# Kernel tuning notes

Hardware: AMD Instinct MI355X
Metric: run time of the kernel (lower is better)

Reference implementation:

```python
import jax, jax.numpy as jnp
import numpy as np

N_ITERS = 10
LAMBDA0 = 0.01


def skew(p):
    # p: (..., 3) -> (..., 3, 3) skew-symmetric matrices
    x, y, z = p[..., 0], p[..., 1], p[..., 2]
    O = jnp.zeros_like(x)
    return jnp.stack([O, -z, y, z, O, -x, -y, x, O], -1).reshape(p.shape[:-1] + (3, 3))


def so3exp(w):
    # Rodrigues formula for a single (3,) rotation vector
    theta2 = jnp.sum(w * w)
    theta = jnp.sqrt(theta2 + 1e-24)
    small = theta < 1e-4
    a = jnp.where(small, 1.0 - theta2 / 6.0, jnp.sin(theta) / theta)
    b = jnp.where(small, 0.5 - theta2 / 24.0, (1.0 - jnp.cos(theta)) / (theta2 + 1e-24))
    W = skew(w)
    return jnp.eye(3, dtype=w.dtype) + a * W + b * (W @ W)


def gather_feats(fm, p2, width, height):
    # fm: (C, Hf, Wf); p2: (N, 2) int pixel coords (x, y). Mirrors indexing_ with
    # flipped points: row = floor(y*Hf/height), col = floor(x*Wf/width).
    Hf, Wf = fm.shape[1], fm.shape[2]
    rows = jnp.clip((p2[:, 1] * Hf) // height, 0, Hf - 1)
    cols = jnp.clip((p2[:, 0] * Wf) // width, 0, Wf - 1)
    return fm[:, rows, cols].T  # (N, C)


def project(pts3D, R, t, K):
    p3 = pts3D @ R.T + t                                  # (N, 3) camera frame
    proj = p3 @ K.T
    xy = jnp.clip(proj[:, :2] / proj[:, 2:3], -1e6, 1e6)  # from_homogeneous
    p2 = jnp.round(xy).astype(jnp.int32) - 1              # (N, 2) int pixels
    return p3, p2


def support_mask(p2, width, height):
    return (p2[:, 0] >= 0) & (p2[:, 1] >= 0) & (p2[:, 0] < width) & (p2[:, 1] < height)


def masked_mean_cost(fm, feature_ref, p2, mask, width, height):
    err = gather_feats(fm, p2, width, height) - feature_ref
    m = mask.astype(err.dtype)
    c = 0.5 * jnp.sum(err * err, -1) * m
    return jnp.sum(c) / jnp.maximum(jnp.sum(m), 1.0)


def setup_inputs():
    key = jax.random.key(0)
    ks = jax.random.split(key, 7)
    N, C, Hf, Wf = 50000, 128, 480, 640
    z = jax.random.uniform(ks[0], (N,), minval=4.0, maxval=8.0)
    x = jax.random.uniform(ks[1], (N,), minval=-0.4, maxval=0.4) * z
    y = jax.random.uniform(ks[2], (N,), minval=-0.3, maxval=0.3) * z
    pts3D = jnp.stack([x, y, z], -1).astype(jnp.float32)
    feature_map_query = jax.random.normal(ks[3], (C, Hf, Wf), jnp.float32)
    feature_grad_x = 0.1 * jax.random.normal(ks[4], (C, Hf, Wf), jnp.float32)
    feature_grad_y = 0.1 * jax.random.normal(ks[5], (C, Hf, Wf), jnp.float32)
    feature_ref = jax.random.normal(ks[6], (N, C), jnp.float32)
    K = jnp.array([[600.0, 0.0, 320.0], [0.0, 600.0, 240.0], [0.0, 0.0, 1.0]], jnp.float32)
    R_init = jnp.eye(3, dtype=jnp.float32)
    t_init = jnp.array([0.1, 0.1, 0.0], jnp.float32)
    return dict(pts3D=pts3D, feature_ref=feature_ref, feature_map_query=feature_map_query,
                feature_grad_x=feature_grad_x, feature_grad_y=feature_grad_y, K=K,
                R_init=R_init, t_init=t_init, im_width=640, im_height=480)


def reference(pts3D, feature_ref, feature_map_query, feature_grad_x, feature_grad_y,
              K, R_init, t_init, im_width, im_height):
    N = pts3D.shape[0]
    fx, fy = K[0, 0], K[1, 1]
    R, t = R_init, t_init
    lam = jnp.asarray(LAMBDA0, pts3D.dtype)
    lr = jnp.asarray(1.0, pts3D.dtype)
    lr_reset = 1.0

    # initial cost (prev_cost at iteration 0 in the original)
    _, p2_0 = project(pts3D, R, t, K)
    mask0 = support_mask(p2_0, im_width, im_height)
    prev_cost = masked_mean_cost(feature_map_query, feature_ref, p2_0, mask0, im_width, im_height)

    eyeN = jnp.broadcast_to(jnp.eye(3, dtype=pts3D.dtype), (N, 3, 3))

    for _ in range(N_ITERS):
        p3, p2 = project(pts3D, R, t, K)
        mask = support_mask(p2, im_width, im_height)
        m = mask.astype(pts3D.dtype)

        err = gather_feats(feature_map_query, p2, im_width, im_height) - feature_ref  # (N, C)

        Z = p3[:, 2]
        Zs = jnp.where(jnp.abs(Z) > 1e-6, Z, 1e-6)  # guard masked-out points only
        # J_p_T: d p3 / d [t, w]  -> (N, 3, 6)
        J_p_T = jnp.concatenate([eyeN, -skew(p3)], -1)
        o = jnp.ones_like(Zs)
        zz = jnp.zeros_like(Zs)
        # J_px_p: d pixel / d p3 -> (N, 2, 3)
        J_px_p = jnp.stack([fx * o, zz, -fx * p3[:, 0] / Zs,
                            zz, fy * o, -fy * p3[:, 1] / Zs], -1).reshape(N, 2, 3) / Zs[:, None, None]
        gx = gather_feats(feature_grad_x, p2, im_width, im_height)  # (N, C)
        gy = gather_feats(feature_grad_y, p2, im_width, im_height)
        J_f_px = jnp.stack([gx, gy], -1)            # (N, C, 2)
        J = J_f_px @ (J_px_p @ J_p_T)               # (N, C, 6)
        Jm = J * m[:, None, None]                   # zero out unsupported points

        Grad = jnp.einsum('ncj,nc->j', Jm, err)     # (6,)
        Hess = jnp.einsum('nck,ncl->kl', Jm, Jm)    # (6, 6)

        Hd = Hess + lam * jnp.diag(jnp.diagonal(Hess) + 1e-9)
        delta = -lr * (jnp.linalg.inv(Hd) @ Grad)
        dt, dw = delta[:3], delta[3:6]
        dr = so3exp(dw)
        R_new = dr @ R
        t_new = dr @ t + dt

        _, p2n = project(pts3D, R_new, t_new, K)
        maskn = support_mask(p2n, im_width, im_height)
        new_cost = masked_mean_cost(feature_map_query, feature_ref, p2n, maskn, im_width, im_height)

        accept = new_cost <= prev_cost
        lam = jnp.clip(lam * jnp.where(accept, 0.1, 10.0), 1e-6, 1e4)
        lr = jnp.where(accept, lr_reset, jnp.clip(0.1 * lr, 1e-3, 1.0))
        R = jnp.where(accept, R_new, R)
        t = jnp.where(accept, t_new, t)
        prev_cost = jnp.where(accept, new_cost, prev_cost)

    return R, t
```

## Files before the change

### kernel.cpp

```cpp
#include <hip/hip_runtime.h>
#include <math.h>

#define NCH 128
#define IMW 640
#define IMH 480
#define HW (IMW * IMH)
#define THREADS 512
#define WPB (THREADS / 64)
#define GBLK 512
#define TSTRIDE (3 * NCH)

#define S_R    0
#define S_T    9
#define S_RC   12
#define S_TC   21
#define S_LAM  24
#define S_LR   25
#define S_PREV 26
#define S_G    32
#define S_TOTAL 64

#define PCOLS 29

struct ProjR {
  float x, y, z;
  int pix;
  bool m;
};

__device__ __forceinline__ ProjR project_pt(const float* __restrict__ pts, int n,
                                            const float R[9], const float T[3],
                                            const float Kv[9]) {
  float px = pts[3 * n + 0], py = pts[3 * n + 1], pz = pts[3 * n + 2];
  ProjR o;
  o.x = R[0] * px + R[1] * py + R[2] * pz + T[0];
  o.y = R[3] * px + R[4] * py + R[5] * pz + T[1];
  o.z = R[6] * px + R[7] * py + R[8] * pz + T[2];
  float pr0 = Kv[0] * o.x + Kv[1] * o.y + Kv[2] * o.z;
  float pr1 = Kv[3] * o.x + Kv[4] * o.y + Kv[5] * o.z;
  float pr2 = Kv[6] * o.x + Kv[7] * o.y + Kv[8] * o.z;
  float u = fminf(fmaxf(pr0 / pr2, -1000000.0f), 1000000.0f);
  float v = fminf(fmaxf(pr1 / pr2, -1000000.0f), 1000000.0f);
  int p2x = (int)rintf(u) - 1;
  int p2y = (int)rintf(v) - 1;
  o.m = (p2x >= 0) && (p2y >= 0) && (p2x < IMW) && (p2y < IMH);
  int r = min(max(p2y, 0), IMH - 1);
  int c = min(max(p2x, 0), IMW - 1);
  o.pix = r * IMW + c;
  return o;
}

__device__ __forceinline__ void jac_rows(const ProjR& p, float fx, float fy,
                                         float A0[6], float A1[6]) {
  float Zs = (fabsf(p.z) > 1e-6f) ? p.z : 1e-6f;
  float iz = 1.0f / Zs;
  float j00 = fx * iz;
  float j02 = -fx * p.x * iz * iz;
  float j11 = fy * iz;
  float j12 = -fy * p.y * iz * iz;
  A0[0] = j00; A0[1] = 0.0f; A0[2] = j02;
  A0[3] = j02 * p.y; A0[4] = j00 * p.z - j02 * p.x; A0[5] = -j00 * p.y;
  A1[0] = 0.0f; A1[1] = j11; A1[2] = j12;
  A1[3] = -j11 * p.z + j12 * p.y; A1[4] = -j12 * p.x; A1[5] = j11 * p.x;
}

__global__ void init_kernel(const float* __restrict__ Rin,
                            const float* __restrict__ tin,
                            double* __restrict__ st) {
  int i = threadIdx.x;
  if (i < 9) { st[S_R + i] = (double)Rin[i]; st[S_RC + i] = (double)Rin[i]; }
  if (i < 3) { st[S_T + i] = (double)tin[i]; st[S_TC + i] = (double)tin[i]; }
  if (i == 0) { st[S_LAM] = 0.01; st[S_LR] = 1.0; st[S_PREV] = 0.0; }
}

__global__ __launch_bounds__(256) void transpose3_kernel(
    const float* __restrict__ f, const float* __restrict__ gx,
    const float* __restrict__ gy, float* __restrict__ t) {
  __shared__ float4 tile4[64][32];
  const int map = blockIdx.y;
  const float* in = (map == 0) ? f : (map == 1) ? gx : gy;
  const int pix0 = blockIdx.x * 64;
#pragma unroll
  for (int mm = 0; mm < 8; ++mm) {
    int k = threadIdx.x + 256 * mm;
    int c  = k >> 4;
    int p4 = (k & 15) * 4;
    float4 v = ((const float4*)(in + (size_t)c * HW + pix0))[k & 15];
    int sw = (c >> 2) ^ (k & 15);
    int e  = c & 3;
    ((float*)&tile4[p4 + 0][sw])[e] = v.x;
    ((float*)&tile4[p4 + 1][sw])[e] = v.y;
    ((float*)&tile4[p4 + 2][sw])[e] = v.z;
    ((float*)&tile4[p4 + 3][sw])[e] = v.w;
  }
  __syncthreads();
#pragma unroll
  for (int mm = 0; mm < 8; ++mm) {
    int k = threadIdx.x + 256 * mm;
    int px = k >> 5;
    int c4 = k & 31;
    float4 v = tile4[px][c4 ^ (px >> 2)];
    ((float4*)(t + (size_t)(pix0 + px) * TSTRIDE + (size_t)map * NCH))[c4] = v;
  }
}

template <bool TRANS>
__global__ __launch_bounds__(THREADS) void fused_kernel(
    const float* __restrict__ pts, const float* __restrict__ fref,
    const float* __restrict__ mf, const float* __restrict__ mgx,
    const float* __restrict__ mgy, const float* __restrict__ Kmat,
    const double* __restrict__ st, double* __restrict__ part, int N) {
  const int lane = threadIdx.x & 63;
  const int wib  = threadIdx.x >> 6;
  const int gw = blockIdx.x * WPB + wib;
  const int nw = gridDim.x * WPB;
  const int half = lane >> 5;
  const int hl   = lane & 31;

  float R[9], T[3], Kv[9];
#pragma unroll
  for (int i = 0; i < 9; ++i) { R[i] = (float)st[S_RC + i]; Kv[i] = Kmat[i]; }
#pragma unroll
  for (int i = 0; i < 3; ++i) T[i] = (float)st[S_TC + i];
  const float fx = Kv[0], fy = Kv[4];

  float hacc[27];
#pragma unroll
  for (int j = 0; j < 27; ++j) hacc[j] = 0.0f;
  double csum = 0.0;
  float cntf = 0.0f;

  for (int base = gw * 2; base < N; base += 2 * nw) {
    const int n = base + half;
    const int nc = min(n, N - 1);
    ProjR p = project_pt(pts, nc, R, T, Kv);
    const float m = (p.m && n < N) ? 1.0f : 0.0f;
    if (__all(m == 0.0f)) continue;

    float A0[6], A1[6];
    jac_rows(p, fx, fy, A0, A1);

    float e0, e1, e2, e3;
    float gxx, gxy, gyy, gxe, gye;
    if (TRANS) {
      const float4* t4 = (const float4*)mf;
      const size_t b = (size_t)p.pix * (TSTRIDE / 4) + hl;
      float4 fv = t4[b];
      float4 gv = t4[b + 32];
      float4 hv = t4[b + 64];
      float4 rv = ((const float4*)fref)[(size_t)nc * (NCH / 4) + hl];
      e0 = fv.x - rv.x; e1 = fv.y - rv.y; e2 = fv.z - rv.z; e3 = fv.w - rv.w;
      gxx = gv.x * gv.x + gv.y * gv.y + gv.z * gv.z + gv.w * gv.w;
      gxy = gv.x * hv.x + gv.y * hv.y + gv.z * hv.z + gv.w * hv.w;
      gyy = hv.x * hv.x + hv.y * hv.y + hv.z * hv.z + hv.w * hv.w;
      gxe = gv.x * e0 + gv.y * e1 + gv.z * e2 + gv.w * e3;
      gye = hv.x * e0 + hv.y * e1 + hv.z * e2 + hv.w * e3;
    } else {
      const int c0 = hl * 4;
      const size_t bb = (size_t)p.pix;
      float f0 = mf[(size_t)(c0 + 0) * HW + bb];
      float f1 = mf[(size_t)(c0 + 1) * HW + bb];
      float f2 = mf[(size_t)(c0 + 2) * HW + bb];
      float f3 = mf[(size_t)(c0 + 3) * HW + bb];
      float gx0 = mgx[(size_t)(c0 + 0) * HW + bb];
      float gx1 = mgx[(size_t)(c0 + 1) * HW + bb];
      float gx2 = mgx[(size_t)(c0 + 2) * HW + bb];
      float gx3 = mgx[(size_t)(c0 + 3) * HW + bb];
      float gy0 = mgy[(size_t)(c0 + 0) * HW + bb];
      float gy1 = mgy[(size_t)(c0 + 1) * HW + bb];
      float gy2 = mgy[(size_t)(c0 + 2) * HW + bb];
      float gy3 = mgy[(size_t)(c0 + 3) * HW + bb];
      float4 rv = ((const float4*)fref)[(size_t)nc * (NCH / 4) + hl];
      e0 = f0 - rv.x; e1 = f1 - rv.y; e2 = f2 - rv.z; e3 = f3 - rv.w;
      gxx = gx0 * gx0 + gx1 * gx1 + gx2 * gx2 + gx3 * gx3;
      gxy = gx0 * gy0 + gx1 * gy1 + gx2 * gy2 + gx3 * gy3;
      gyy = gy0 * gy0 + gy1 * gy1 + gy2 * gy2 + gy3 * gy3;
      gxe = gx0 * e0 + gx1 * e1 + gx2 * e2 + gx3 * e3;
      gye = gy0 * e0 + gy1 * e1 + gy2 * e2 + gy3 * e3;
    }

    gxx *= m; gxy *= m; gyy *= m; gxe *= m; gye *= m;
    csum += (double)(m * (e0 * e0 + e1 * e1 + e2 * e2 + e3 * e3));
    if (hl == 0) cntf += m;

#pragma unroll
    for (int k = 0; k < 6; ++k) hacc[k] += gxe * A0[k] + gye * A1[k];
    float u[6], v[6];
#pragma unroll
    for (int k = 0; k < 6; ++k) {
      u[k] = gxx * A0[k] + gxy * A1[k];
      v[k] = gxy * A0[k] + gyy * A1[k];
    }
    int q = 6;
#pragma unroll
    for (int k = 0; k < 6; ++k)
#pragma unroll
      for (int l = k; l < 6; ++l) {
        hacc[q] += u[k] * A0[l] + v[k] * A1[l];
        ++q;
      }
  }

  __shared__ double red[WPB][PCOLS];
#pragma unroll
  for (int j = 0; j < 27; ++j) {
    double d = (double)hacc[j];
#pragma unroll
    for (int off = 32; off > 0; off >>= 1) d += __shfl_xor(d, off);
    if (lane == 0) red[wib][j] = d;
  }
  {
    double cs = csum;
    float cf = cntf;
#pragma unroll
    for (int off = 32; off > 0; off >>= 1) {
      cs += __shfl_xor(cs, off);
      cf += __shfl_xor(cf, off);
    }
    if (lane == 0) { red[wib][27] = cs; red[wib][28] = (double)cf; }
  }
  __syncthreads();
  if (wib == 0 && lane < PCOLS) {
    double s = 0.0;
#pragma unroll
    for (int w = 0; w < WPB; ++w) s += red[w][lane];
    part[(size_t)blockIdx.x * PCOLS + lane] = s;
  }
}

__global__ void update_solve_kernel(const double* __restrict__ part, int GB,
                                    double* __restrict__ st,
                                    float* __restrict__ out, int is_init) {
  __shared__ double red[16][PCOLS];
  __shared__ double tot[PCOLS];
  int q = threadIdx.x & 31;
  int chunk = threadIdx.x >> 5;
  if (q < PCOLS) {
    double s = 0.0;
    for (int b = chunk; b < GB; b += 16) s += part[(size_t)b * PCOLS + q];
    red[chunk][q] = s;
  }
  __syncthreads();
  if (threadIdx.x < PCOLS) {
    double t = 0.0;
#pragma unroll
    for (int ch = 0; ch < 16; ++ch) t += red[ch][threadIdx.x];
    tot[threadIdx.x] = t;
  }
  __syncthreads();
  if (threadIdx.x == 0) {
    double nc = 0.5 * tot[27] / fmax(tot[28], 1.0);
    bool accept;
    if (is_init) {
      accept = true;
      st[S_PREV] = nc;
    } else {
      accept = (nc <= st[S_PREV]);
      double lam = st[S_LAM] * (accept ? 0.1 : 10.0);
      st[S_LAM] = fmin(fmax(lam, 1e-6), 1e4);
      st[S_LR] = accept ? 1.0 : fmin(fmax(0.1 * st[S_LR], 1e-3), 1.0);
      if (accept) st[S_PREV] = nc;
    }
    if (accept) {
      for (int i = 0; i < 9; ++i) st[S_R + i] = st[S_RC + i];
      for (int i = 0; i < 3; ++i) st[S_T + i] = st[S_TC + i];
      for (int j = 0; j < 27; ++j) st[S_G + j] = tot[j];
    }
    for (int i = 0; i < 9; ++i) out[i] = (float)st[S_R + i];
    for (int i = 0; i < 3; ++i) out[9 + i] = (float)st[S_T + i];

    double Grad[6], Hs[6][6];
    for (int j = 0; j < 6; ++j) Grad[j] = st[S_G + j];
    int qq = 0;
    for (int k = 0; k < 6; ++k)
      for (int l = k; l < 6; ++l) { Hs[k][l] = Hs[l][k] = st[S_G + 6 + qq]; ++qq; }
    double lam = st[S_LAM], lr = st[S_LR];
    double M[6][7];
    for (int i = 0; i < 6; ++i) {
      for (int j = 0; j < 6; ++j) M[i][j] = Hs[i][j];
      M[i][i] += lam * (Hs[i][i] + 1e-9);
      M[i][6] = Grad[i];
    }
    for (int c = 0; c < 6; ++c) {
      int piv = c;
      double mx = fabs(M[c][c]);
      for (int r = c + 1; r < 6; ++r) {
        double a = fabs(M[r][c]);
        if (a > mx) { mx = a; piv = r; }
      }
      if (piv != c)
        for (int j = 0; j < 7; ++j) {
          double tmp = M[c][j]; M[c][j] = M[piv][j]; M[piv][j] = tmp;
        }
      double pv = M[c][c];
      if (pv == 0.0) pv = 1e-30;
      for (int r = c + 1; r < 6; ++r) {
        double f = M[r][c] / pv;
        for (int j = c; j < 7; ++j) M[r][j] -= f * M[c][j];
      }
    }
    double xs[6];
    for (int i = 5; i >= 0; --i) {
      double v = M[i][6];
      for (int j = i + 1; j < 6; ++j) v -= M[i][j] * xs[j];
      double pv = M[i][i];
      if (pv == 0.0) pv = 1e-30;
      xs[i] = v / pv;
    }
    double dt[3] = {-lr * xs[0], -lr * xs[1], -lr * xs[2]};
    double dw[3] = {-lr * xs[3], -lr * xs[4], -lr * xs[5]};
    double th2 = dw[0] * dw[0] + dw[1] * dw[1] + dw[2] * dw[2];
    double th = sqrt(th2 + 1e-24);
    double a, b;
    if (th < 1e-4) { a = 1.0 - th2 / 6.0; b = 0.5 - th2 / 24.0; }
    else { a = sin(th) / th; b = (1.0 - cos(th)) / (th2 + 1e-24); }
    double W[3][3] = {{0, -dw[2], dw[1]}, {dw[2], 0, -dw[0]}, {-dw[1], dw[0], 0}};
    double W2[3][3];
    for (int i = 0; i < 3; ++i)
      for (int j = 0; j < 3; ++j) {
        double s = 0.0;
        for (int k = 0; k < 3; ++k) s += W[i][k] * W[k][j];
        W2[i][j] = s;
      }
    double dr[3][3];
    for (int i = 0; i < 3; ++i)
      for (int j = 0; j < 3; ++j)
        dr[i][j] = ((i == j) ? 1.0 : 0.0) + a * W[i][j] + b * W2[i][j];
    for (int i = 0; i < 3; ++i) {
      for (int j = 0; j < 3; ++j) {
        double s = 0.0;
        for (int k = 0; k < 3; ++k) s += dr[i][k] * st[S_R + k * 3 + j];
        st[S_RC + i * 3 + j] = s;
      }
      double s = 0.0;
      for (int k = 0; k < 3; ++k) s += dr[i][k] * st[S_T + k];
      st[S_TC + i] = s + dt[i];
    }
  }
}

extern "C" void kernel_launch(void* const* d_in, const int* in_sizes, int n_in,
                              void* d_out, int out_size, void* d_ws, size_t ws_size,
                              hipStream_t stream) {
  const float* pts  = (const float*)d_in[0];
  const float* fref = (const float*)d_in[1];
  const float* fm   = (const float*)d_in[2];
  const float* gxm  = (const float*)d_in[3];
  const float* gym  = (const float*)d_in[4];
  const float* Kmat = (const float*)d_in[5];
  const float* Rin  = (const float*)d_in[6];
  const float* tin  = (const float*)d_in[7];
  const int N = in_sizes[0] / 3;

  double* st = (double*)d_ws;
  double* part = st + S_TOTAL;
  float* out = (float*)d_out;

  const size_t state_doubles = S_TOTAL + (size_t)GBLK * PCOLS;
  const size_t map_floats = (size_t)HW * NCH;
  const size_t need_fast =
      state_doubles * sizeof(double) + 3 * map_floats * sizeof(float) + 256;

  init_kernel<<<1, 64, 0, stream>>>(Rin, tin, st);

  if (ws_size >= need_fast) {
    float* tmap = (float*)(st + state_doubles);
    transpose3_kernel<<<dim3(HW / 64, 3), 256, 0, stream>>>(fm, gxm, gym, tmap);
    fused_kernel<true><<<GBLK, THREADS, 0, stream>>>(pts, fref, tmap, tmap, tmap,
                                                     Kmat, st, part, N);
    update_solve_kernel<<<1, 512, 0, stream>>>(part, GBLK, st, out, 1);
    for (int it = 0; it < 10; ++it) {
      fused_kernel<true><<<GBLK, THREADS, 0, stream>>>(pts, fref, tmap, tmap,
                                                       tmap, Kmat, st, part, N);
      update_solve_kernel<<<1, 512, 0, stream>>>(part, GBLK, st, out, 0);
    }
  } else {
    fused_kernel<false><<<GBLK, THREADS, 0, stream>>>(pts, fref, fm, gxm, gym,
                                                      Kmat, st, part, N);
    update_solve_kernel<<<1, 512, 0, stream>>>(part, GBLK, st, out, 1);
    for (int it = 0; it < 10; ++it) {
      fused_kernel<false><<<GBLK, THREADS, 0, stream>>>(pts, fref, fm, gxm, gym,
                                                        Kmat, st, part, N);
      update_solve_kernel<<<1, 512, 0, stream>>>(part, GBLK, st, out, 0);
    }
  }
}
```

Measured before the change: 1.033 ms.

## Sort points by projected pixel bucket to improve gather locality

Adds a counting sort (key, scan, scatter kernels) that orders points by their initial projected pixel bucket, and the fused kernel iterates through this order. The aim is for neighbouring waves to gather nearby rows of the transposed feature maps, improving cache hit rates. It also flattens the transpose grid so the three maps interleave. The cost is three extra launches, an indirection on each point, and scattered reads of points and reference features.

After: 1.064 ms. 1.03x slower.

```diff
diff --git a/kernel.cpp b/kernel.cpp
--- a/kernel.cpp
+++ b/kernel.cpp
@@ -9,6 +9,7 @@
 #define WPB (THREADS / 64)
 #define GBLK 512
 #define TSTRIDE (3 * NCH)
+#define NBUCK (HW / 64)
 
 #define S_R    0
 #define S_T    9
@@ -66,20 +67,80 @@
 
 __global__ void init_kernel(const float* __restrict__ Rin,
                             const float* __restrict__ tin,
-                            double* __restrict__ st) {
-  int i = threadIdx.x;
-  if (i < 9) { st[S_R + i] = (double)Rin[i]; st[S_RC + i] = (double)Rin[i]; }
-  if (i < 3) { st[S_T + i] = (double)tin[i]; st[S_TC + i] = (double)tin[i]; }
-  if (i == 0) { st[S_LAM] = 0.01; st[S_LR] = 1.0; st[S_PREV] = 0.0; }
+                            double* __restrict__ st, int* __restrict__ hist) {
+  if (blockIdx.x == 0) {
+    int i = threadIdx.x;
+    if (i < 9) { st[S_R + i] = (double)Rin[i]; st[S_RC + i] = (double)Rin[i]; }
+    if (i < 3) { st[S_T + i] = (double)tin[i]; st[S_TC + i] = (double)tin[i]; }
+    if (i == 0) { st[S_LAM] = 0.01; st[S_LR] = 1.0; st[S_PREV] = 0.0; }
+  }
+  int gid = blockIdx.x * blockDim.x + threadIdx.x;
+  for (int i = gid; i < NBUCK; i += gridDim.x * blockDim.x) hist[i] = 0;
+}
+
+__global__ __launch_bounds__(256) void sort_key_kernel(
+    const float* __restrict__ pts, const float* __restrict__ Rin,
+    const float* __restrict__ tin, const float* __restrict__ Kmat,
+    int* __restrict__ keys, int* __restrict__ hist, int N) {
+  int n = blockIdx.x * 256 + threadIdx.x;
+  if (n >= N) return;
+  float R[9], T[3], Kv[9];
+#pragma unroll
+  for (int i = 0; i < 9; ++i) { R[i] = Rin[i]; Kv[i] = Kmat[i]; }
+#pragma unroll
+  for (int i = 0; i < 3; ++i) T[i] = tin[i];
+  ProjR p = project_pt(pts, n, R, T, Kv);
+  keys[n] = p.pix;
+  atomicAdd(&hist[p.pix >> 6], 1);
+}
+
+__global__ __launch_bounds__(512) void sort_scan_kernel(
+    const int* __restrict__ hist, int* __restrict__ offs) {
+  __shared__ int tsum[512];
+  const int C = (NBUCK + 511) / 512;
+  int t = threadIdx.x;
+  int local[C];
+  int s = 0;
+#pragma unroll
+  for (int j = 0; j < C; ++j) {
+    int idx = t * C + j;
+    int v = (idx < NBUCK) ? hist[idx] : 0;
+    local[j] = s;
+    s += v;
+  }
+  tsum[t] = s;
+  __syncthreads();
+  for (int off = 1; off < 512; off <<= 1) {
+    int y = (t >= off) ? tsum[t - off] : 0;
+    __syncthreads();
+    tsum[t] += y;
+    __syncthreads();
+  }
+  int base = (t == 0) ? 0 : tsum[t - 1];
+#pragma unroll
+  for (int j = 0; j < C; ++j) {
+    int idx = t * C + j;
+    if (idx < NBUCK) offs[idx] = base + local[j];
+  }
+}
+
+__global__ __launch_bounds__(256) void sort_scatter_kernel(
+    const int* __restrict__ keys, int* __restrict__ offs,
+    int* __restrict__ order, int N) {
+  int n = blockIdx.x * 256 + threadIdx.x;
+  if (n >= N) return;
+  int b = keys[n] >> 6;
+  int pos = atomicAdd(&offs[b], 1);
+  order[pos] = n;
 }
 
 __global__ __launch_bounds__(256) void transpose3_kernel(
     const float* __restrict__ f, const float* __restrict__ gx,
     const float* __restrict__ gy, float* __restrict__ t) {
   __shared__ float4 tile4[64][32];
-  const int map = blockIdx.y;
+  const int map = blockIdx.x % 3;
+  const int pix0 = (blockIdx.x / 3) * 64;
   const float* in = (map == 0) ? f : (map == 1) ? gx : gy;
-  const int pix0 = blockIdx.x * 64;
 #pragma unroll
   for (int mm = 0; mm < 8; ++mm) {
     int k = threadIdx.x + 256 * mm;
@@ -109,6 +170,7 @@
     const float* __restrict__ pts, const float* __restrict__ fref,
     const float* __restrict__ mf, const float* __restrict__ mgx,
     const float* __restrict__ mgy, const float* __restrict__ Kmat,
+    const int* __restrict__ order,
     const double* __restrict__ st, double* __restrict__ part, int N) {
   const int lane = threadIdx.x & 63;
   const int wib  = threadIdx.x >> 6;
@@ -131,10 +193,10 @@
   float cntf = 0.0f;
 
   for (int base = gw * 2; base < N; base += 2 * nw) {
-    const int n = base + half;
-    const int nc = min(n, N - 1);
-    ProjR p = project_pt(pts, nc, R, T, Kv);
-    const float m = (p.m && n < N) ? 1.0f : 0.0f;
+    const int i = base + half;
+    const int n = order[min(i, N - 1)];
+    ProjR p = project_pt(pts, n, R, T, Kv);
+    const float m = (p.m && i < N) ? 1.0f : 0.0f;
     if (__all(m == 0.0f)) continue;
 
     float A0[6], A1[6];
@@ -148,7 +210,7 @@
       float4 fv = t4[b];
       float4 gv = t4[b + 32];
       float4 hv = t4[b + 64];
-      float4 rv = ((const float4*)fref)[(size_t)nc * (NCH / 4) + hl];
+      float4 rv = ((const float4*)fref)[(size_t)n * (NCH / 4) + hl];
       e0 = fv.x - rv.x; e1 = fv.y - rv.y; e2 = fv.z - rv.z; e3 = fv.w - rv.w;
       gxx = gv.x * gv.x + gv.y * gv.y + gv.z * gv.z + gv.w * gv.w;
       gxy = gv.x * hv.x + gv.y * hv.y + gv.z * hv.z + gv.w * hv.w;
@@ -170,7 +232,7 @@
       float gy1 = mgy[(size_t)(c0 + 1) * HW + bb];
       float gy2 = mgy[(size_t)(c0 + 2) * HW + bb];
       float gy3 = mgy[(size_t)(c0 + 3) * HW + bb];
-      float4 rv = ((const float4*)fref)[(size_t)nc * (NCH / 4) + hl];
+      float4 rv = ((const float4*)fref)[(size_t)n * (NCH / 4) + hl];
       e0 = f0 - rv.x; e1 = f1 - rv.y; e2 = f2 - rv.z; e3 = f3 - rv.w;
       gxx = gx0 * gx0 + gx1 * gx1 + gx2 * gx2 + gx3 * gx3;
       gxy = gx0 * gy0 + gx1 * gy1 + gx2 * gy2 + gx3 * gy3;
@@ -354,33 +416,45 @@
 
   double* st = (double*)d_ws;
   double* part = st + S_TOTAL;
+  int* keys  = (int*)(part + (size_t)GBLK * PCOLS);
+  int* order = keys + N;
+  int* hist  = order + N;
+  int* offs  = hist + NBUCK;
+  size_t int_end = (size_t)((char*)(offs + NBUCK) - (char*)d_ws);
+  size_t tmap_off = (int_end + 15) & ~(size_t)15;
+  float* tmap = (float*)((char*)d_ws + tmap_off);
   float* out = (float*)d_out;
 
-  const size_t state_doubles = S_TOTAL + (size_t)GBLK * PCOLS;
   const size_t map_floats = (size_t)HW * NCH;
-  const size_t need_fast =
-      state_doubles * sizeof(double) + 3 * map_floats * sizeof(float) + 256;
-
-  init_kernel<<<1, 64, 0, stream>>>(Rin, tin, st);
+  const size_t need_fast = tmap_off + 3 * map_floats * sizeof(float) + 256;
+  const int npb = (N + 255) / 256;
+
+  init_kernel<<<10, 512, 0, stream>>>(Rin, tin, st, hist);
 
   if (ws_size >= need_fast) {
-    float* tmap = (float*)(st + state_doubles);
-    transpose3_kernel<<<dim3(HW / 64, 3), 256, 0, stream>>>(fm, gxm, gym, tmap);
+    sort_key_kernel<<<npb, 256, 0, stream>>>(pts, Rin, tin, Kmat, keys, hist, N);
+    sort_scan_kernel<<<1, 512, 0, stream>>>(hist, offs);
+    sort_scatter_kernel<<<npb, 256, 0, stream>>>(keys, offs, order, N);
+    transpose3_kernel<<<(HW / 64) * 3, 256, 0, stream>>>(fm, gxm, gym, tmap);
     fused_kernel<true><<<GBLK, THREADS, 0, stream>>>(pts, fref, tmap, tmap, tmap,
-                                                     Kmat, st, part, N);
+                                                     Kmat, order, st, part, N);
     update_solve_kernel<<<1, 512, 0, stream>>>(part, GBLK, st, out, 1);
     for (int it = 0; it < 10; ++it) {
       fused_kernel<true><<<GBLK, THREADS, 0, stream>>>(pts, fref, tmap, tmap,
-                                                       tmap, Kmat, st, part, N);
+                                                       tmap, Kmat, order, st,
+                                                       part, N);
       update_solve_kernel<<<1, 512, 0, stream>>>(part, GBLK, st, out, 0);
     }
   } else {
+    sort_key_kernel<<<npb, 256, 0, stream>>>(pts, Rin, tin, Kmat, keys, hist, N);
+    sort_scan_kernel<<<1, 512, 0, stream>>>(hist, offs);
+    sort_scatter_kernel<<<npb, 256, 0, stream>>>(keys, offs, order, N);
     fused_kernel<false><<<GBLK, THREADS, 0, stream>>>(pts, fref, fm, gxm, gym,
-                                                      Kmat, st, part, N);
+                                                      Kmat, order, st, part, N);
     update_solve_kernel<<<1, 512, 0, stream>>>(part, GBLK, st, out, 1);
     for (int it = 0; it < 10; ++it) {
       fused_kernel<false><<<GBLK, THREADS, 0, stream>>>(pts, fref, fm, gxm, gym,
-                                                        Kmat, st, part, N);
+                                                        Kmat, order, st, part, N);
       update_solve_kernel<<<1, 512, 0, stream>>>(part, GBLK, st, out, 0);
     }
   }
```

## Fold solve into fused kernel via last-block atomic reduction; retile transpose

Applied to the files above, without the earlier changes.

Removes the separate update_solve kernel: each block of the fused kernel publishes its partial sums, and an atomic counter picks the last-arriving block, which does the final reduction and the 6x6 LM solve/update in place. This cuts 11 kernel launches and their inter-kernel gaps. The transpose kernel is also rewritten to handle all three maps per 32-pixel tile with 512 threads, an interleaved tile order and a new LDS swizzle, aiming for better read coalescing and contiguous writes. The risks are in the atomic/fence ordering, and in the serial solve tail that now runs inside the fused kernel.

After: 1.486 ms. +43.8%, slower.

```diff
diff --git a/kernel.cpp b/kernel.cpp
--- a/kernel.cpp
+++ b/kernel.cpp
@@ -9,6 +9,8 @@
 #define WPB (THREADS / 64)
 #define GBLK 512
 #define TSTRIDE (3 * NCH)
+#define TPX 32
+#define NTILE (HW / TPX)
 
 #define S_R    0
 #define S_T    9
@@ -21,6 +23,7 @@
 #define S_TOTAL 64
 
 #define PCOLS 29
+#define PSTRIDE 32
 
 struct ProjR {
   float x, y, z;
@@ -66,41 +69,53 @@
 
 __global__ void init_kernel(const float* __restrict__ Rin,
                             const float* __restrict__ tin,
-                            double* __restrict__ st) {
+                            double* __restrict__ st, int* __restrict__ cnt) {
   int i = threadIdx.x;
   if (i < 9) { st[S_R + i] = (double)Rin[i]; st[S_RC + i] = (double)Rin[i]; }
   if (i < 3) { st[S_T + i] = (double)tin[i]; st[S_TC + i] = (double)tin[i]; }
   if (i == 0) { st[S_LAM] = 0.01; st[S_LR] = 1.0; st[S_PREV] = 0.0; }
-}
-
-__global__ __launch_bounds__(256) void transpose3_kernel(
+  if (i < 16) cnt[i] = 0;
+}
+
+__global__ __launch_bounds__(512) void transpose3_kernel(
     const float* __restrict__ f, const float* __restrict__ gx,
     const float* __restrict__ gy, float* __restrict__ t) {
-  __shared__ float4 tile4[64][32];
-  const int map = blockIdx.y;
-  const float* in = (map == 0) ? f : (map == 1) ? gx : gy;
-  const int pix0 = blockIdx.x * 64;
-#pragma unroll
-  for (int mm = 0; mm < 8; ++mm) {
-    int k = threadIdx.x + 256 * mm;
-    int c  = k >> 4;
-    int p4 = (k & 15) * 4;
-    float4 v = ((const float4*)(in + (size_t)c * HW + pix0))[k & 15];
-    int sw = (c >> 2) ^ (k & 15);
-    int e  = c & 3;
-    ((float*)&tile4[p4 + 0][sw])[e] = v.x;
-    ((float*)&tile4[p4 + 1][sw])[e] = v.y;
-    ((float*)&tile4[p4 + 2][sw])[e] = v.z;
-    ((float*)&tile4[p4 + 3][sw])[e] = v.w;
+  __shared__ float4 l4[TPX * 96];
+  const int bx = blockIdx.x;
+  const int tile = (bx & 7) * (NTILE / 8) + (bx >> 3);
+  const int pix0 = tile * TPX;
+
+  float4 v[6];
+#pragma unroll
+  for (int it = 0; it < 6; ++it) {
+    int k = threadIdx.x + 512 * it;
+    int map = k >> 10;
+    int r = k & 1023;
+    int c = r >> 3;
+    int g = r & 7;
+    const float* in = (map == 0) ? f : (map == 1) ? gx : gy;
+    v[it] = ((const float4*)(in + (size_t)c * HW + pix0))[g];
+  }
+#pragma unroll
+  for (int it = 0; it < 6; ++it) {
+    int k = threadIdx.x + 512 * it;
+    int map = k >> 10;
+    int r = k & 1023;
+    int c = r >> 3, g = r & 7;
+    int j = map * 32 + (c >> 2), e = c & 3;
+    int jb = j ^ g;
+    ((float*)&l4[(4 * g + 0) * 96 + (jb ^ 0)])[e] = v[it].x;
+    ((float*)&l4[(4 * g + 1) * 96 + (jb ^ 1)])[e] = v[it].y;
+    ((float*)&l4[(4 * g + 2) * 96 + (jb ^ 2)])[e] = v[it].z;
+    ((float*)&l4[(4 * g + 3) * 96 + (jb ^ 3)])[e] = v[it].w;
   }
   __syncthreads();
 #pragma unroll
-  for (int mm = 0; mm < 8; ++mm) {
-    int k = threadIdx.x + 256 * mm;
-    int px = k >> 5;
-    int c4 = k & 31;
-    float4 v = tile4[px][c4 ^ (px >> 2)];
-    ((float4*)(t + (size_t)(pix0 + px) * TSTRIDE + (size_t)map * NCH))[c4] = v;
+  for (int it = 0; it < 6; ++it) {
+    int o = threadIdx.x + 512 * it;
+    int px = o / 96, j = o % 96;
+    float4 w = l4[px * 96 + (j ^ ((px >> 2) & 7) ^ (px & 3))];
+    ((float4*)t)[(size_t)pix0 * 96 + o] = w;
   }
 }
 
@@ -109,7 +124,8 @@
     const float* __restrict__ pts, const float* __restrict__ fref,
     const float* __restrict__ mf, const float* __restrict__ mgx,
     const float* __restrict__ mgy, const float* __restrict__ Kmat,
-    const double* __restrict__ st, double* __restrict__ part, int N) {
+    double* __restrict__ st, double* __restrict__ part, int* __restrict__ cnt,
+    float* __restrict__ out, int N, int pass) {
   const int lane = threadIdx.x & 63;
   const int wib  = threadIdx.x >> 6;
   const int gw = blockIdx.x * WPB + wib;
@@ -131,24 +147,22 @@
   float cntf = 0.0f;
 
   for (int base = gw * 2; base < N; base += 2 * nw) {
-    const int n = base + half;
-    const int nc = min(n, N - 1);
-    ProjR p = project_pt(pts, nc, R, T, Kv);
-    const float m = (p.m && n < N) ? 1.0f : 0.0f;
+    const int n = min(base + half, N - 1);
+    ProjR p = project_pt(pts, n, R, T, Kv);
+    const float m = (p.m && (base + half) < N) ? 1.0f : 0.0f;
     if (__all(m == 0.0f)) continue;
 
     float A0[6], A1[6];
     jac_rows(p, fx, fy, A0, A1);
 
-    float e0, e1, e2, e3;
-    float gxx, gxy, gyy, gxe, gye;
+    float e0, e1, e2, e3, gxx, gxy, gyy, gxe, gye;
     if (TRANS) {
       const float4* t4 = (const float4*)mf;
-      const size_t b = (size_t)p.pix * (TSTRIDE / 4) + hl;
+      const size_t b = (size_t)p.pix * 96 + hl;
       float4 fv = t4[b];
       float4 gv = t4[b + 32];
       float4 hv = t4[b + 64];
-      float4 rv = ((const float4*)fref)[(size_t)nc * (NCH / 4) + hl];
+      float4 rv = ((const float4*)fref)[(size_t)n * (NCH / 4) + hl];
       e0 = fv.x - rv.x; e1 = fv.y - rv.y; e2 = fv.z - rv.z; e3 = fv.w - rv.w;
       gxx = gv.x * gv.x + gv.y * gv.y + gv.z * gv.z + gv.w * gv.w;
       gxy = gv.x * hv.x + gv.y * hv.y + gv.z * hv.z + gv.w * hv.w;
@@ -170,7 +184,7 @@
       float gy1 = mgy[(size_t)(c0 + 1) * HW + bb];
       float gy2 = mgy[(size_t)(c0 + 2) * HW + bb];
       float gy3 = mgy[(size_t)(c0 + 3) * HW + bb];
-      float4 rv = ((const float4*)fref)[(size_t)nc * (NCH / 4) + hl];
+      float4 rv = ((const float4*)fref)[(size_t)n * (NCH / 4) + hl];
       e0 = f0 - rv.x; e1 = f1 - rv.y; e2 = f2 - rv.z; e3 = f3 - rv.w;
       gxx = gx0 * gx0 + gx1 * gx1 + gx2 * gx2 + gx3 * gx3;
       gxy = gx0 * gy0 + gx1 * gy1 + gx2 * gy2 + gx3 * gy3;
@@ -220,38 +234,53 @@
     if (lane == 0) { red[wib][27] = cs; red[wib][28] = (double)cf; }
   }
   __syncthreads();
-  if (wib == 0 && lane < PCOLS) {
-    double s = 0.0;
-#pragma unroll
-    for (int w = 0; w < WPB; ++w) s += red[w][lane];
-    part[(size_t)blockIdx.x * PCOLS + lane] = s;
-  }
-}
-
-__global__ void update_solve_kernel(const double* __restrict__ part, int GB,
-                                    double* __restrict__ st,
-                                    float* __restrict__ out, int is_init) {
-  __shared__ double red[16][PCOLS];
+
+  __shared__ int is_last_s;
+  if (wib == 0) {
+    if (lane < PCOLS) {
+      double s = 0.0;
+#pragma unroll
+      for (int w = 0; w < WPB; ++w) s += red[w][lane];
+      __hip_atomic_store(&part[(size_t)blockIdx.x * PSTRIDE + lane], s,
+                         __ATOMIC_RELAXED, __HIP_MEMORY_SCOPE_AGENT);
+    }
+    __threadfence();
+    if (lane == 0) {
+      int old = __hip_atomic_fetch_add(&cnt[pass], 1, __ATOMIC_ACQ_REL,
+                                       __HIP_MEMORY_SCOPE_AGENT);
+      is_last_s = (old == (int)gridDim.x - 1) ? 1 : 0;
+    }
+  }
+  __syncthreads();
+  if (!is_last_s) return;
+
+  __shared__ double redf[16][PCOLS];
   __shared__ double tot[PCOLS];
-  int q = threadIdx.x & 31;
-  int chunk = threadIdx.x >> 5;
-  if (q < PCOLS) {
-    double s = 0.0;
-    for (int b = chunk; b < GB; b += 16) s += part[(size_t)b * PCOLS + q];
-    red[chunk][q] = s;
+  {
+    int q = threadIdx.x & 31;
+    int chunk = threadIdx.x >> 5;
+    if (q < PCOLS) {
+      double s = 0.0;
+      for (int b = chunk; b < (int)gridDim.x; b += 16)
+        s += __hip_atomic_load(&part[(size_t)b * PSTRIDE + q],
+                               __ATOMIC_RELAXED, __HIP_MEMORY_SCOPE_AGENT);
+      redf[chunk][q] = s;
+    }
   }
   __syncthreads();
   if (threadIdx.x < PCOLS) {
-    double t = 0.0;
-#pragma unroll
-    for (int ch = 0; ch < 16; ++ch) t += red[ch][threadIdx.x];
-    tot[threadIdx.x] = t;
+    double s = 0.0;
+#pragma unroll
+    for (int ch = 0; ch < 16; ++ch) s += redf[ch][threadIdx.x];
+    tot[threadIdx.x] = s;
   }
   __syncthreads();
-  if (threadIdx.x == 0) {
+  if (threadIdx.x != 0) return;
+
+  {
     double nc = 0.5 * tot[27] / fmax(tot[28], 1.0);
     bool accept;
-    if (is_init) {
+    if (pass == 0) {
       accept = true;
       st[S_PREV] = nc;
     } else {
@@ -295,17 +324,17 @@
       double pv = M[c][c];
       if (pv == 0.0) pv = 1e-30;
       for (int r = c + 1; r < 6; ++r) {
-        double f = M[r][c] / pv;
-        for (int j = c; j < 7; ++j) M[r][j] -= f * M[c][j];
+        double fq = M[r][c] / pv;
+        for (int j = c; j < 7; ++j) M[r][j] -= fq * M[c][j];
       }
     }
     double xs[6];
     for (int i = 5; i >= 0; --i) {
-      double v = M[i][6];
-      for (int j = i + 1; j < 6; ++j) v -= M[i][j] * xs[j];
+      double vv = M[i][6];
+      for (int j = i + 1; j < 6; ++j) vv -= M[i][j] * xs[j];
       double pv = M[i][i];
       if (pv == 0.0) pv = 1e-30;
-      xs[i] = v / pv;
+      xs[i] = vv / pv;
     }
     double dt[3] = {-lr * xs[0], -lr * xs[1], -lr * xs[2]};
     double dw[3] = {-lr * xs[3], -lr * xs[4], -lr * xs[5]};
@@ -354,34 +383,27 @@
 
   double* st = (double*)d_ws;
   double* part = st + S_TOTAL;
+  int* cnt = (int*)(part + (size_t)GBLK * PSTRIDE);
+  size_t int_end = (size_t)((char*)(cnt + 16) - (char*)d_ws);
+  size_t tmap_off = (int_end + 15) & ~(size_t)15;
+  float* tmap = (float*)((char*)d_ws + tmap_off);
   float* out = (float*)d_out;
 
-  const size_t state_doubles = S_TOTAL + (size_t)GBLK * PCOLS;
   const size_t map_floats = (size_t)HW * NCH;
-  const size_t need_fast =
-      state_doubles * sizeof(double) + 3 * map_floats * sizeof(float) + 256;
-
-  init_kernel<<<1, 64, 0, stream>>>(Rin, tin, st);
+  const size_t need_fast = tmap_off + 3 * map_floats * sizeof(float) + 256;
+
+  init_kernel<<<1, 512, 0, stream>>>(Rin, tin, st, cnt);
 
   if (ws_size >= need_fast) {
-    float* tmap = (float*)(st + state_doubles);
-    transpose3_kernel<<<dim3(HW / 64, 3), 256, 0, stream>>>(fm, gxm, gym, tmap);
-    fused_kernel<true><<<GBLK, THREADS, 0, stream>>>(pts, fref, tmap, tmap, tmap,
-                                                     Kmat, st, part, N);
-    update_solve_kernel<<<1, 512, 0, stream>>>(part, GBLK, st, out, 1);
-    for (int it = 0; it < 10; ++it) {
-      fused_kernel<true><<<GBLK, THREADS, 0, stream>>>(pts, fref, tmap, tmap,
-                                                       tmap, Kmat, st, part, N);
-      update_solve_kernel<<<1, 512, 0, stream>>>(part, GBLK, st, out, 0);
+    transpose3_kernel<<<NTILE, 512, 0, stream>>>(fm, gxm, gym, tmap);
+    for (int pass = 0; pass < 11; ++pass) {
+      fused_kernel<true><<<GBLK, THREADS, 0, stream>>>(
+          pts, fref, tmap, tmap, tmap, Kmat, st, part, cnt, out, N, pass);
     }
   } else {
-    fused_kernel<false><<<GBLK, THREADS, 0, stream>>>(pts, fref, fm, gxm, gym,
-                                                      Kmat, st, part, N);
-    update_solve_kernel<<<1, 512, 0, stream>>>(part, GBLK, st, out, 1);
-    for (int it = 0; it < 10; ++it) {
-      fused_kernel<false><<<GBLK, THREADS, 0, stream>>>(pts, fref, fm, gxm, gym,
-                                                        Kmat, st, part, N);
-      update_solve_kernel<<<1, 512, 0, stream>>>(part, GBLK, st, out, 0);
-    }
-  }
-}
+    for (int pass = 0; pass < 11; ++pass) {
+      fused_kernel<false><<<GBLK, THREADS, 0, stream>>>(
+          pts, fref, fm, gxm, gym, Kmat, st, part, cnt, out, N, pass);
+    }
+  }
+}
```
